# Kernel optimization log

Measured on AMD Instinct MI355X. Metric: run time of the kernel, lower is better.

The kernel has to match this reference:

```python
import jax, jax.numpy as jnp
import numpy as np

N, C, T, V, K = 64, 64, 300, 25, 3
EPS = 1e-5


def setup_inputs() -> dict:
    key = jax.random.key(0)
    ks = jax.random.split(key, 4)
    x = jax.random.normal(ks[0], (N, C, T, V), dtype=jnp.float32)
    A = jax.random.uniform(ks[1], (K, V, V), dtype=jnp.float32)
    # per-subset 1x1 conv weights: W[k] maps C_in -> C_out, plus bias b[k]
    W = jax.random.normal(ks[2], (K, C, C), dtype=jnp.float32) * (1.0 / np.sqrt(C))
    b = jax.random.normal(ks[3], (K, C), dtype=jnp.float32) * 0.01
    gamma = jnp.ones((C,), dtype=jnp.float32)
    beta = jnp.zeros((C,), dtype=jnp.float32)
    return {"x": x, "A": A, "W": W, "b": b, "gamma": gamma, "beta": beta}


def reference(x, A, W, b, gamma, beta):
    # y = sum_k conv1x1_k( einsum('nctv,vw->nctw', x, A[k]) )
    # conv1x1 over (C,T,V) with kernel 1 == channel matmul; fuse subsets via one einsum.
    y = jnp.einsum('nctv,kvw,koc->notw', x, A, W)
    y = y + jnp.sum(b, axis=0)[None, :, None, None]
    # BatchNorm2d in training mode: batch statistics over (N, T, V) per channel
    mean = jnp.mean(y, axis=(0, 2, 3), keepdims=True)
    var = jnp.mean(jnp.square(y - mean), axis=(0, 2, 3), keepdims=True)
    y = gamma[None, :, None, None] * (y - mean) * jax.lax.rsqrt(var + EPS) + beta[None, :, None, None]
    # residual (in_channels == out_channels -> identity) + relu
    return jax.nn.relu(y + x)
```

## Files before the change

kernel.cpp:

```cpp
#include <hip/hip_runtime.h>
#include <hip/hip_bf16.h>

#define N_ 64
#define C_ 64
#define T_ 300
#define V_ 25
#define K_ 3
#define TT 6
#define NTILE 50
#define NBLK 3200
#define NPERS 1024
#define XROW 192
#define WP 72
#define ATP 40
#define NTHR 512
#define EPS_ 1e-5f

typedef __bf16 bf16_t;
typedef __bf16 bf16x4 __attribute__((ext_vector_type(4)));
typedef __bf16 bf16x8 __attribute__((ext_vector_type(8)));
typedef float f32x4 __attribute__((ext_vector_type(4)));
typedef float f32x4u __attribute__((ext_vector_type(4), aligned(4)));

static __device__ __forceinline__ bf16_t tobf(float f) { return (bf16_t)f; }
static __device__ __forceinline__ int emask(int c) { return ((c & 3) << 3) | ((c & 8) << 2); }

union SmemU {
  struct { bf16_t W[3 * 64 * WP]; bf16_t At[3 * 32 * ATP]; } wa;
  bf16_t xs[64 * XROW];
};

struct Frags {
  bf16x8 wfrag[6];
  bf16x8 afrag[3][2];
  int fK[4], fS5[4];
  float bs[4];
  int obase;
};

static __device__ __forceinline__ void stage_wa(
    const float* __restrict__ A, const float* __restrict__ W, SmemU& sm, int tid) {
  for (int m = tid; m < 3072; m += NTHR) {
    f32x4 v4 = *(reinterpret_cast<const f32x4*>(W) + m);
    int f = m << 2;
    int k = f >> 12, o = (f >> 6) & 63, c = f & 63;
    bf16x4 h;
    h[0] = tobf(v4[0]); h[1] = tobf(v4[1]); h[2] = tobf(v4[2]); h[3] = tobf(v4[3]);
    *reinterpret_cast<bf16x4*>(&sm.wa.W[(k * 64 + o) * WP + c]) = h;
  }
  for (int i = tid; i < 3072; i += NTHR) {
    int k = i >> 10, r = i & 1023, w = r >> 5, v = r & 31;
    float val = (v < V_ && w < V_) ? A[k * 625 + v * 25 + w] : 0.f;
    sm.wa.At[(k * 32 + w) * ATP + v] = tobf(val);
  }
}

static __device__ __forceinline__ void read_frags(
    const SmemU& sm, const float* __restrict__ b, int ob, int l15, int lg, Frags& F) {
  const int o = ob * 16 + l15;
  #pragma unroll
  for (int k = 0; k < 3; ++k)
    #pragma unroll
    for (int ch = 0; ch < 2; ++ch)
      F.wfrag[k * 2 + ch] =
          *reinterpret_cast<const bf16x8*>(&sm.wa.W[(k * 64 + o) * WP + ch * 32 + lg * 8]);
  #pragma unroll
  for (int k = 0; k < 3; ++k)
    #pragma unroll
    for (int wh = 0; wh < 2; ++wh)
      F.afrag[k][wh] =
          *reinterpret_cast<const bf16x8*>(&sm.wa.At[(k * 32 + wh * 16 + l15) * ATP + lg * 8]);
  const int crow = 8 * (l15 >> 2) + (l15 & 3);
  #pragma unroll
  for (int q = 0; q < 4; ++q) {
    int c = ((q >> 1) * 32) + ((q & 1) * 4) + crow;
    int em = emask(c);
    F.fK[q] = c * XROW + ((lg * 8) ^ (em & 24));
    F.fS5[q] = em & 32;
  }
  F.obase = ob * 16 + lg * 4;
  #pragma unroll
  for (int r = 0; r < 4; ++r)
    F.bs[r] = b[F.obase + r] + b[64 + F.obase + r] + b[128 + F.obase + r];
}

static __device__ __forceinline__ void stage_x(
    const float* __restrict__ x, SmemU& sm, int n, int t0, int tid) {
  const int c = tid >> 3, vb = tid & 7;
  const int em = emask(c);
  const float* xr = x + (size_t)n * 480000 + (size_t)c * 7500 + (size_t)t0 * 25;
  bf16_t* xsr = &sm.xs[c * XROW];
  #pragma unroll
  for (int t = 0; t < TT; ++t) {
    bf16x4 h;
    if (vb < 6) {
      f32x4u v4 = *reinterpret_cast<const f32x4u*>(xr + t * 25 + vb * 4);
      h[0] = tobf(v4[0]); h[1] = tobf(v4[1]); h[2] = tobf(v4[2]); h[3] = tobf(v4[3]);
    } else if (vb == 6) {
      float s = xr[t * 25 + 24];
      h[0] = tobf(s); h[1] = tobf(0.f); h[2] = tobf(0.f); h[3] = tobf(0.f);
    } else {
      h[0] = tobf(0.f); h[1] = tobf(0.f); h[2] = tobf(0.f); h[3] = tobf(0.f);
    }
    *reinterpret_cast<bf16x4*>(&xsr[(((t << 5) + vb * 4) ^ em)]) = h;
  }
}

static __device__ __forceinline__ void compute_wh(
    const bf16x8* xf, const Frags& F, int wh, f32x4& acc0, f32x4& acc1) {
  acc0 = f32x4{0.f, 0.f, 0.f, 0.f};
  acc1 = f32x4{0.f, 0.f, 0.f, 0.f};
  #pragma unroll
  for (int k = 0; k < 3; ++k) {
    #pragma unroll
    for (int ch = 0; ch < 2; ++ch) {
      f32x4 zero = {0.f, 0.f, 0.f, 0.f};
      f32x4 dP = __builtin_amdgcn_mfma_f32_16x16x32_bf16(xf[ch * 2 + 0], F.afrag[k][wh], zero, 0, 0, 0);
      f32x4 dQ = __builtin_amdgcn_mfma_f32_16x16x32_bf16(xf[ch * 2 + 1], F.afrag[k][wh], zero, 0, 0, 0);
      bf16x8 zf;
      zf[0] = tobf(dP[0]); zf[1] = tobf(dP[1]); zf[2] = tobf(dP[2]); zf[3] = tobf(dP[3]);
      zf[4] = tobf(dQ[0]); zf[5] = tobf(dQ[1]); zf[6] = tobf(dQ[2]); zf[7] = tobf(dQ[3]);
      if (ch == 0)
        acc0 = __builtin_amdgcn_mfma_f32_16x16x32_bf16(F.wfrag[k * 2 + ch], zf, acc0, 0, 0, 0);
      else
        acc1 = __builtin_amdgcn_mfma_f32_16x16x32_bf16(F.wfrag[k * 2 + ch], zf, acc1, 0, 0, 0);
    }
  }
}

__global__ __launch_bounds__(NTHR, 4) void k1_compute(
    const float* __restrict__ x, const float* __restrict__ A,
    const float* __restrict__ W, const float* __restrict__ b,
    float* __restrict__ y, float* __restrict__ part, int* __restrict__ counter) {
  __shared__ __align__(16) SmemU sm;
  __shared__ float stats2[2][2][64];
  __shared__ int tile_s;

  const int tid = threadIdx.x;
  const int lane = tid & 63;
  const int wv = tid >> 6;
  const int ob = wv & 3;
  const int th = wv >> 2;
  const int l15 = lane & 15;
  const int lg = lane >> 4;

  stage_wa(A, W, sm, tid);
  __syncthreads();
  Frags F;
  read_frags(sm, b, ob, l15, lg, F);

  const int w_lo = l15, w_hi = 16 + l15;

  for (;;) {
    if (tid == 0) tile_s = atomicAdd(counter, 1);
    __syncthreads();
    const int tile = tile_s;
    if (tile >= NBLK) break;
    const int n = tile / NTILE;
    const int t0 = (tile - n * NTILE) * TT;

    stage_x(x, sm, n, t0, tid);
    __syncthreads();

    float lsum[4] = {0.f, 0.f, 0.f, 0.f}, lsq[4] = {0.f, 0.f, 0.f, 0.f};
    float* yb = y + (size_t)n * 480000 + (size_t)t0 * 25;

    #pragma unroll
    for (int tl = 0; tl < 3; ++tl) {
      const int t = th * 3 + tl;
      bf16x8 xf[4];
      #pragma unroll
      for (int q = 0; q < 4; ++q)
        xf[q] = *reinterpret_cast<const bf16x8*>(sm.xs + F.fK[q] + ((t << 5) ^ F.fS5[q]));
      #pragma unroll
      for (int wh = 0; wh < 2; ++wh) {
        f32x4 acc0, acc1;
        compute_wh(xf, F, wh, acc0, acc1);
        const int w = wh ? w_hi : w_lo;
        if (w < V_) {
          #pragma unroll
          for (int r = 0; r < 4; ++r) {
            float val = acc0[r] + acc1[r] + F.bs[r];
            lsum[r] += val;
            lsq[r] += val * val;
            yb[(size_t)(F.obase + r) * 7500 + t * 25 + w] = val;
          }
        }
      }
    }

    #pragma unroll
    for (int d = 1; d < 16; d <<= 1) {
      #pragma unroll
      for (int r = 0; r < 4; ++r) {
        lsum[r] += __shfl_xor(lsum[r], d);
        lsq[r]  += __shfl_xor(lsq[r], d);
      }
    }
    if (l15 == 0) {
      #pragma unroll
      for (int r = 0; r < 4; ++r) {
        stats2[0][th][F.obase + r] = lsum[r];
        stats2[1][th][F.obase + r] = lsq[r];
      }
    }
    __syncthreads();
    if (tid < 128)
      part[(size_t)tile * 128 + tid] =
          stats2[tid >> 6][0][tid & 63] + stats2[tid >> 6][1][tid & 63];
  }
}

__global__ __launch_bounds__(256) void k2_stats(
    const float* __restrict__ part,
    const float* __restrict__ gamma, const float* __restrict__ beta,
    float* __restrict__ ss) {
  const int o = blockIdx.x;
  const int tid = threadIdx.x;
  double s = 0.0, q = 0.0;
  for (int i = tid; i < NBLK; i += 256) {
    s += (double)part[(size_t)i * 128 + o];
    q += (double)part[(size_t)i * 128 + 64 + o];
  }
  __shared__ double sd[256], qd[256];
  sd[tid] = s; qd[tid] = q;
  __syncthreads();
  for (int step = 128; step > 0; step >>= 1) {
    if (tid < step) { sd[tid] += sd[tid + step]; qd[tid] += qd[tid + step]; }
    __syncthreads();
  }
  if (tid == 0) {
    const double cnt = 480000.0;
    double mean = sd[0] / cnt;
    double var = qd[0] / cnt - mean * mean;
    float inv = rsqrtf((float)var + EPS_);
    float sc = gamma[o] * inv;
    float sh = beta[o] - (float)mean * sc;
    ss[2 * o] = sc;
    ss[2 * o + 1] = sh;
  }
}

__global__ __launch_bounds__(256) void k3_finish(
    const float* __restrict__ x, const float* __restrict__ ss,
    float* __restrict__ y) {
  const int p = blockIdx.x;
  const int c = p & 63;
  const float sc = ss[2 * c];
  const float sh = ss[2 * c + 1];
  const float4* xv = reinterpret_cast<const float4*>(x + (size_t)p * 7500);
  float4* yv = reinterpret_cast<float4*>(y + (size_t)p * 7500);
  for (int i = threadIdx.x; i < 1875; i += 256) {
    float4 a = yv[i];
    float4 b4 = xv[i];
    float4 o;
    o.x = fmaxf(sc * a.x + sh + b4.x, 0.f);
    o.y = fmaxf(sc * a.y + sh + b4.y, 0.f);
    o.z = fmaxf(sc * a.z + sh + b4.z, 0.f);
    o.w = fmaxf(sc * a.w + sh + b4.w, 0.f);
    yv[i] = o;
  }
}

extern "C" void kernel_launch(void* const* d_in, const int* in_sizes, int n_in,
                              void* d_out, int out_size, void* d_ws, size_t ws_size,
                              hipStream_t stream) {
  const float* x     = (const float*)d_in[0];
  const float* A     = (const float*)d_in[1];
  const float* W     = (const float*)d_in[2];
  const float* b     = (const float*)d_in[3];
  const float* gamma = (const float*)d_in[4];
  const float* beta  = (const float*)d_in[5];
  float* y = (float*)d_out;

  int*   counter = (int*)d_ws;
  float* part = (float*)d_ws + 64;
  float* ss   = part + (size_t)NBLK * 128;

  hipMemsetAsync(counter, 0, sizeof(int), stream);
  k1_compute<<<NPERS, NTHR, 0, stream>>>(x, A, W, b, y, part, counter);
  k2_stats<<<64, 256, 0, stream>>>(part, gamma, beta, ss);
  k3_finish<<<4096, 256, 0, stream>>>(x, ss, y);
}
```

Before: 160.9 us.

## Double-buffer x tiles with register prefetch and static tile assignment

Replaces the atomic work counter with a static round-robin assignment of tiles to the 1024 persistent blocks. The next tile's x values are loaded into registers while the current tile is computed, then written into a second LDS buffer, which drops one barrier per tile. BN partial sums now accumulate across all of a block's tiles and are written once per block, so k2 reads fewer partials and the memset launch goes away. In exchange the kernel uses more LDS and registers, which may lower occupancy, and the static split loses dynamic load balancing.

```diff
diff --git a/kernel.cpp b/kernel.cpp
--- a/kernel.cpp
+++ b/kernel.cpp
@@ -11,6 +11,7 @@
 #define NBLK 3200
 #define NPERS 1024
 #define XROW 192
+#define XBUF (64 * XROW)
 #define WP 72
 #define ATP 40
 #define NTHR 512
@@ -27,7 +28,7 @@
 
 union SmemU {
   struct { bf16_t W[3 * 64 * WP]; bf16_t At[3 * 32 * ATP]; } wa;
-  bf16_t xs[64 * XROW];
+  bf16_t xs[2 * XBUF];
 };
 
 struct Frags {
@@ -84,21 +85,33 @@
     F.bs[r] = b[F.obase + r] + b[64 + F.obase + r] + b[128 + F.obase + r];
 }
 
-static __device__ __forceinline__ void stage_x(
-    const float* __restrict__ x, SmemU& sm, int n, int t0, int tid) {
-  const int c = tid >> 3, vb = tid & 7;
-  const int em = emask(c);
+static __device__ __forceinline__ void prefetch_issue(
+    f32x4u* pv, const float* __restrict__ x, int tile, int c, int vb) {
+  const int n = tile / NTILE;
+  const int t0 = (tile - n * NTILE) * TT;
   const float* xr = x + (size_t)n * 480000 + (size_t)c * 7500 + (size_t)t0 * 25;
-  bf16_t* xsr = &sm.xs[c * XROW];
+  if (vb < 6) {
+    #pragma unroll
+    for (int t = 0; t < TT; ++t)
+      pv[t] = *reinterpret_cast<const f32x4u*>(xr + t * 25 + vb * 4);
+  } else if (vb == 6) {
+    #pragma unroll
+    for (int t = 0; t < TT; ++t)
+      pv[t][0] = xr[t * 25 + 24];
+  }
+}
+
+static __device__ __forceinline__ void stage_write(
+    const f32x4u* pv, bf16_t* xsbuf, int c, int vb, int em) {
+  bf16_t* xsr = xsbuf + c * XROW;
   #pragma unroll
   for (int t = 0; t < TT; ++t) {
     bf16x4 h;
     if (vb < 6) {
-      f32x4u v4 = *reinterpret_cast<const f32x4u*>(xr + t * 25 + vb * 4);
-      h[0] = tobf(v4[0]); h[1] = tobf(v4[1]); h[2] = tobf(v4[2]); h[3] = tobf(v4[3]);
+      h[0] = tobf(pv[t][0]); h[1] = tobf(pv[t][1]);
+      h[2] = tobf(pv[t][2]); h[3] = tobf(pv[t][3]);
     } else if (vb == 6) {
-      float s = xr[t * 25 + 24];
-      h[0] = tobf(s); h[1] = tobf(0.f); h[2] = tobf(0.f); h[3] = tobf(0.f);
+      h[0] = tobf(pv[t][0]); h[1] = tobf(0.f); h[2] = tobf(0.f); h[3] = tobf(0.f);
     } else {
       h[0] = tobf(0.f); h[1] = tobf(0.f); h[2] = tobf(0.f); h[3] = tobf(0.f);
     }
@@ -131,11 +144,11 @@
 __global__ __launch_bounds__(NTHR, 4) void k1_compute(
     const float* __restrict__ x, const float* __restrict__ A,
     const float* __restrict__ W, const float* __restrict__ b,
-    float* __restrict__ y, float* __restrict__ part, int* __restrict__ counter) {
+    float* __restrict__ y, float* __restrict__ part) {
   __shared__ __align__(16) SmemU sm;
   __shared__ float stats2[2][2][64];
-  __shared__ int tile_s;
-
+
+  const int bid = blockIdx.x;
   const int tid = threadIdx.x;
   const int lane = tid & 63;
   const int wv = tid >> 6;
@@ -143,26 +156,34 @@
   const int th = wv >> 2;
   const int l15 = lane & 15;
   const int lg = lane >> 4;
+  const int c = tid >> 3, vb = tid & 7;
+  const int em = emask(c);
 
   stage_wa(A, W, sm, tid);
   __syncthreads();
   Frags F;
   read_frags(sm, b, ob, l15, lg, F);
-
+  __syncthreads();
+
+  const int nt = (bid < (NBLK - 3 * NPERS)) ? 4 : 3;
   const int w_lo = l15, w_hi = 16 + l15;
 
-  for (;;) {
-    if (tid == 0) tile_s = atomicAdd(counter, 1);
-    __syncthreads();
-    const int tile = tile_s;
-    if (tile >= NBLK) break;
+  float lsum[4] = {0.f, 0.f, 0.f, 0.f}, lsq[4] = {0.f, 0.f, 0.f, 0.f};
+  f32x4u pv[TT];
+
+  prefetch_issue(pv, x, bid, c, vb);
+  stage_write(pv, sm.xs, c, vb, em);
+  __syncthreads();
+
+  int cur = 0;
+  for (int i = 0; i < nt; ++i) {
+    const int tile = bid + i * NPERS;
     const int n = tile / NTILE;
     const int t0 = (tile - n * NTILE) * TT;
 
-    stage_x(x, sm, n, t0, tid);
-    __syncthreads();
-
-    float lsum[4] = {0.f, 0.f, 0.f, 0.f}, lsq[4] = {0.f, 0.f, 0.f, 0.f};
+    if (i + 1 < nt) prefetch_issue(pv, x, tile + NPERS, c, vb);
+
+    const bf16_t* xsc = sm.xs + cur * XBUF;
     float* yb = y + (size_t)n * 480000 + (size_t)t0 * 25;
 
     #pragma unroll
@@ -171,7 +192,7 @@
       bf16x8 xf[4];
       #pragma unroll
       for (int q = 0; q < 4; ++q)
-        xf[q] = *reinterpret_cast<const bf16x8*>(sm.xs + F.fK[q] + ((t << 5) ^ F.fS5[q]));
+        xf[q] = *reinterpret_cast<const bf16x8*>(xsc + F.fK[q] + ((t << 5) ^ F.fS5[q]));
       #pragma unroll
       for (int wh = 0; wh < 2; ++wh) {
         f32x4 acc0, acc1;
@@ -189,26 +210,30 @@
       }
     }
 
-    #pragma unroll
-    for (int d = 1; d < 16; d <<= 1) {
-      #pragma unroll
-      for (int r = 0; r < 4; ++r) {
-        lsum[r] += __shfl_xor(lsum[r], d);
-        lsq[r]  += __shfl_xor(lsq[r], d);
-      }
-    }
-    if (l15 == 0) {
-      #pragma unroll
-      for (int r = 0; r < 4; ++r) {
-        stats2[0][th][F.obase + r] = lsum[r];
-        stats2[1][th][F.obase + r] = lsq[r];
-      }
-    }
+    if (i + 1 < nt) stage_write(pv, sm.xs + (cur ^ 1) * XBUF, c, vb, em);
     __syncthreads();
-    if (tid < 128)
-      part[(size_t)tile * 128 + tid] =
-          stats2[tid >> 6][0][tid & 63] + stats2[tid >> 6][1][tid & 63];
-  }
+    cur ^= 1;
+  }
+
+  #pragma unroll
+  for (int d = 1; d < 16; d <<= 1) {
+    #pragma unroll
+    for (int r = 0; r < 4; ++r) {
+      lsum[r] += __shfl_xor(lsum[r], d);
+      lsq[r]  += __shfl_xor(lsq[r], d);
+    }
+  }
+  if (l15 == 0) {
+    #pragma unroll
+    for (int r = 0; r < 4; ++r) {
+      stats2[0][th][F.obase + r] = lsum[r];
+      stats2[1][th][F.obase + r] = lsq[r];
+    }
+  }
+  __syncthreads();
+  if (tid < 128)
+    part[(size_t)bid * 128 + tid] =
+        stats2[tid >> 6][0][tid & 63] + stats2[tid >> 6][1][tid & 63];
 }
 
 __global__ __launch_bounds__(256) void k2_stats(
@@ -218,7 +243,7 @@
   const int o = blockIdx.x;
   const int tid = threadIdx.x;
   double s = 0.0, q = 0.0;
-  for (int i = tid; i < NBLK; i += 256) {
+  for (int i = tid; i < NPERS; i += 256) {
     s += (double)part[(size_t)i * 128 + o];
     q += (double)part[(size_t)i * 128 + 64 + o];
   }
@@ -273,12 +298,10 @@
   const float* beta  = (const float*)d_in[5];
   float* y = (float*)d_out;
 
-  int*   counter = (int*)d_ws;
-  float* part = (float*)d_ws + 64;
-  float* ss   = part + (size_t)NBLK * 128;
-
-  hipMemsetAsync(counter, 0, sizeof(int), stream);
-  k1_compute<<<NPERS, NTHR, 0, stream>>>(x, A, W, b, y, part, counter);
+  float* part = (float*)d_ws;
+  float* ss   = part + (size_t)NPERS * 128;
+
+  k1_compute<<<NPERS, NTHR, 0, stream>>>(x, A, W, b, y, part);
   k2_stats<<<64, 256, 0, stream>>>(part, gamma, beta, ss);
   k3_finish<<<4096, 256, 0, stream>>>(x, ss, y);
 }
```

Result: slower. 196.8 us (+22.3%).
